# Kernel tuning notes

Measured on AMD Instinct MI355X. Metric: run time of the kernel, lower is better.

The kernel has to match this reference:

```python
import jax, jax.numpy as jnp
import numpy as np

K = 8192
D = 512


def setup_inputs() -> dict:
    key = jax.random.key(0)
    k1, k2 = jax.random.split(key)
    x = jax.random.normal(k1, (32, 512, D), dtype=jnp.float32)
    # nn.Embedding weight init: uniform(-1/k, 1/k)
    codebook = jax.random.uniform(k2, (K, D), dtype=jnp.float32,
                                  minval=-1.0 / K, maxval=1.0 / K)
    return {"x": x, "codebook": codebook}


def reference(x, codebook):
    # flatten to [N, D]
    z_e = x.reshape(-1, x.shape[-1])
    # squared L2 distances: ||z||^2 - 2 z c^T + ||c||^2  -> [N, K]
    dists = (jnp.sum(z_e * z_e, axis=1, keepdims=True)
             - 2.0 * jnp.einsum('nd,kd->nk', z_e, codebook)
             + jnp.sum(codebook * codebook, axis=1)[None, :])
    indices = jnp.argmin(dists, axis=1)  # [N]
    z_q = codebook[indices]              # [N, D] gather
    # straight-through estimator: forward z_q, grad passes to z_e
    z_q_st = z_e + jax.lax.stop_gradient(z_q - z_e)
    # vq loss pulls codebook toward (detached) encoder outputs
    vq_loss = jnp.mean((z_q - jax.lax.stop_gradient(z_e)) ** 2)
    # commitment loss pulls encoder outputs toward (detached) codes
    commit_loss = jnp.mean((z_e - jax.lax.stop_gradient(z_q)) ** 2)
    z_q_out = z_q_st.reshape(x.shape)
    idx_out = indices.reshape(x.shape[:-1])
    return z_q_out, vq_loss, commit_loss, idx_out
```

## Files before the change

kernel.cpp:

```cpp
#include <hip/hip_runtime.h>

#define K_CODES 8192
#define D_DIM   512
#define N_ROWS  16384
#define NSPLIT  32
#define CAP     8
#define T2      2.0e-4f
#define LIST_CAP 32768

typedef __attribute__((ext_vector_type(8))) short bf16x8;
typedef __attribute__((ext_vector_type(4))) float f32x4;
typedef unsigned char uchar;
typedef unsigned short ushort;
typedef unsigned long long u64;

__device__ __forceinline__ unsigned fkey(float f) {
    unsigned b = __float_as_uint(f);
    return (b & 0x80000000u) ? ~b : (b | 0x80000000u);
}
__device__ __forceinline__ float finv(unsigned k) {
    return __uint_as_float((k & 0x80000000u) ? (k & 0x7fffffffu) : ~k);
}

__device__ __forceinline__ unsigned pk_bf16(float a, float b) {
    unsigned ua = __float_as_uint(a), ub = __float_as_uint(b);
    ua = (ua + 0x7fffu + ((ua >> 16) & 1u)) >> 16;
    ub = (ub + 0x7fffu + ((ub >> 16) & 1u)) & 0xffff0000u;
    return ua | ub;
}

__global__ void vq_prepass(const float* __restrict__ x, const float* __restrict__ cb,
                           unsigned* __restrict__ xb, unsigned* __restrict__ cbb,
                           float* __restrict__ sn, u64* __restrict__ keys,
                           int* __restrict__ count) {
    const int bid = blockIdx.x;
    const int t = threadIdx.x;
    if (bid < 6144) {
        const size_t gid = (size_t)bid * 256 + t;
        const size_t nx = (size_t)N_ROWS * D_DIM / 8;
        if (gid < nx) {
            const float4 f0 = ((const float4*)x)[gid * 2];
            const float4 f1 = ((const float4*)x)[gid * 2 + 1];
            ((uint4*)xb)[gid] = make_uint4(pk_bf16(f0.x, f0.y), pk_bf16(f0.z, f0.w),
                                           pk_bf16(f1.x, f1.y), pk_bf16(f1.z, f1.w));
        } else {
            const size_t g = gid - nx;
            const float4 f0 = ((const float4*)cb)[g * 2];
            const float4 f1 = ((const float4*)cb)[g * 2 + 1];
            ((uint4*)cbb)[g] = make_uint4(pk_bf16(f0.x, f0.y), pk_bf16(f0.z, f0.w),
                                          pk_bf16(f1.x, f1.y), pk_bf16(f1.z, f1.w));
        }
    } else {
        const int base = (bid - 6144) * 8;
        if (bid == 6144 && t == 0) *count = 0;
        if (t < 8) keys[base + t] = ~0ull;
        const int wave = t >> 6, lane = t & 63;
        const int row = base + wave * 2 + (lane >> 5);
        const int l = lane & 31, b = l >> 3, j = l & 7;
        const float* a = x + (size_t)row * D_DIM + b * 128 + j;
        float r = __fmul_rn(a[0], a[0]);
#pragma unroll
        for (int i = 1; i < 16; ++i) {
            const float v = a[i * 8];
            r = __fadd_rn(r, __fmul_rn(v, v));
        }
        r = __fadd_rn(r, __shfl_xor(r, 1));
        r = __fadd_rn(r, __shfl_xor(r, 2));
        r = __fadd_rn(r, __shfl_xor(r, 4));
        r = __fadd_rn(r, __shfl_xor(r, 8));
        r = __fadd_rn(r, __shfl_xor(r, 16));
        if (l == 0) sn[row] = r;
    }
}

__global__ __launch_bounds__(256)
void vq_sn(const float* __restrict__ x, float* __restrict__ sn,
           u64* __restrict__ keys, int* __restrict__ count) {
    const int t = threadIdx.x;
    const int base = blockIdx.x * 8;
    if (blockIdx.x == 0 && t == 0) *count = 0;
    if (t < 8) keys[base + t] = ~0ull;
    const int wave = t >> 6, lane = t & 63;
    const int row = base + wave * 2 + (lane >> 5);
    const int l = lane & 31, b = l >> 3, j = l & 7;
    const float* a = x + (size_t)row * D_DIM + b * 128 + j;
    float r = __fmul_rn(a[0], a[0]);
#pragma unroll
    for (int i = 1; i < 16; ++i) {
        const float v = a[i * 8];
        r = __fadd_rn(r, __fmul_rn(v, v));
    }
    r = __fadd_rn(r, __shfl_xor(r, 1));
    r = __fadd_rn(r, __shfl_xor(r, 2));
    r = __fadd_rn(r, __shfl_xor(r, 4));
    r = __fadd_rn(r, __shfl_xor(r, 8));
    r = __fadd_rn(r, __shfl_xor(r, 16));
    if (l == 0) sn[row] = r;
}

template<bool PRE>
__global__ __launch_bounds__(256, 2)
void vq_screen2(const float* __restrict__ x, const float* __restrict__ cb,
                const ushort* __restrict__ xb, const ushort* __restrict__ cbb,
                float* __restrict__ g_dmax, uchar* __restrict__ g_cnt,
                uchar* __restrict__ g_cand) {
    __shared__ ushort Ash[128 * 32];
    __shared__ ushort Bsh[256 * 32];
    __shared__ unsigned vkey[128];
    __shared__ int ccnt[128];
    __shared__ uchar clist[128][CAP];

    const int t    = threadIdx.x;
    const int w    = t >> 6, lane = t & 63;
    const int fr   = lane & 15;
    const int quad = lane >> 4;
    const int wr   = (w & 1) * 64;
    const int wc   = (w >> 1) * 128;
    const int row0  = blockIdx.y * 128;
    const int kbase = blockIdx.x * 256;

    if (t < 128) { vkey[t] = 0u; ccnt[t] = 0; }

    const int r = t >> 1, h = t & 1;
    const int sA = (r >> 1) & 3;
    const int ca0 = (2 * h) ^ sA;
    ushort* awp0 = &Ash[r * 32 + ca0 * 8];
    ushort* awp1 = &Ash[r * 32 + (ca0 ^ 1) * 8];
    const int sB = (t >> 1) & 3;
    ushort* bwp0 = &Bsh[t * 32 + (0 ^ sB) * 8];
    ushort* bwp1 = &Bsh[t * 32 + (1 ^ sB) * 8];
    ushort* bwp2 = &Bsh[t * 32 + (2 ^ sB) * 8];
    ushort* bwp3 = &Bsh[t * 32 + (3 ^ sB) * 8];

    int aoff[4], boff[8];
#pragma unroll
    for (int i = 0; i < 4; ++i) {
        const int rw = wr + i * 16 + fr;
        aoff[i] = rw * 32 + ((quad ^ (rw >> 1)) & 3) * 8;
    }
#pragma unroll
    for (int j = 0; j < 8; ++j) {
        const int rw = wc + j * 16 + fr;
        boff[j] = rw * 32 + ((quad ^ (rw >> 1)) & 3) * 8;
    }

    f32x4 acc[4][8];
#pragma unroll
    for (int i = 0; i < 4; ++i)
#pragma unroll
        for (int j = 0; j < 8; ++j) acc[i][j] = (f32x4)0.0f;

    if (PRE) {
        const char* gA = (const char*)(xb  + (size_t)(row0 + r) * D_DIM + h * 16);
        const char* gB = (const char*)(cbb + (size_t)(kbase + t) * D_DIM);
        uint4 a0 = *(const uint4*)(gA);
        uint4 a1 = *(const uint4*)(gA + 16);
        uint4 b0 = *(const uint4*)(gB);
        uint4 b1 = *(const uint4*)(gB + 16);
        uint4 b2 = *(const uint4*)(gB + 32);
        uint4 b3 = *(const uint4*)(gB + 48);
        for (int dc = 0; dc < 16; ++dc) {
            __syncthreads();
            *(uint4*)awp0 = a0; *(uint4*)awp1 = a1;
            *(uint4*)bwp0 = b0; *(uint4*)bwp1 = b1;
            *(uint4*)bwp2 = b2; *(uint4*)bwp3 = b3;
            const int dn = (dc + 1) & 15;
            a0 = *(const uint4*)(gA + dn * 64);
            a1 = *(const uint4*)(gA + dn * 64 + 16);
            b0 = *(const uint4*)(gB + dn * 64);
            b1 = *(const uint4*)(gB + dn * 64 + 16);
            b2 = *(const uint4*)(gB + dn * 64 + 32);
            b3 = *(const uint4*)(gB + dn * 64 + 48);
            __syncthreads();
            bf16x8 af[4], bfv[8];
#pragma unroll
            for (int i = 0; i < 4; ++i) af[i] = *(const bf16x8*)&Ash[aoff[i]];
#pragma unroll
            for (int j = 0; j < 8; ++j) bfv[j] = *(const bf16x8*)&Bsh[boff[j]];
#pragma unroll
            for (int i = 0; i < 4; ++i)
#pragma unroll
                for (int j = 0; j < 8; ++j)
                    acc[i][j] = __builtin_amdgcn_mfma_f32_16x16x32_bf16(af[i], bfv[j], acc[i][j], 0, 0, 0);
        }
    } else {
        const char* gA = (const char*)(x  + (size_t)(row0 + r) * D_DIM + h * 16);
        const char* gB = (const char*)(cb + (size_t)(kbase + t) * D_DIM);
        for (int dc = 0; dc < 16; ++dc) {
            const float4* fa = (const float4*)(gA + dc * 128);
            float4 f0 = fa[0], f1 = fa[1], f2 = fa[2], f3 = fa[3];
            uint4 a0 = make_uint4(pk_bf16(f0.x, f0.y), pk_bf16(f0.z, f0.w),
                                  pk_bf16(f1.x, f1.y), pk_bf16(f1.z, f1.w));
            uint4 a1 = make_uint4(pk_bf16(f2.x, f2.y), pk_bf16(f2.z, f2.w),
                                  pk_bf16(f3.x, f3.y), pk_bf16(f3.z, f3.w));
            const float4* fb = (const float4*)(gB + dc * 128);
            float4 g0 = fb[0], g1 = fb[1], g2 = fb[2], g3 = fb[3];
            float4 g4 = fb[4], g5 = fb[5], g6 = fb[6], g7 = fb[7];
            uint4 b0 = make_uint4(pk_bf16(g0.x, g0.y), pk_bf16(g0.z, g0.w),
                                  pk_bf16(g1.x, g1.y), pk_bf16(g1.z, g1.w));
            uint4 b1 = make_uint4(pk_bf16(g2.x, g2.y), pk_bf16(g2.z, g2.w),
                                  pk_bf16(g3.x, g3.y), pk_bf16(g3.z, g3.w));
            uint4 b2 = make_uint4(pk_bf16(g4.x, g4.y), pk_bf16(g4.z, g4.w),
                                  pk_bf16(g5.x, g5.y), pk_bf16(g5.z, g5.w));
            uint4 b3 = make_uint4(pk_bf16(g6.x, g6.y), pk_bf16(g6.z, g6.w),
                                  pk_bf16(g7.x, g7.y), pk_bf16(g7.z, g7.w));
            __syncthreads();
            *(uint4*)awp0 = a0; *(uint4*)awp1 = a1;
            *(uint4*)bwp0 = b0; *(uint4*)bwp1 = b1;
            *(uint4*)bwp2 = b2; *(uint4*)bwp3 = b3;
            __syncthreads();
            bf16x8 af[4], bfv[8];
#pragma unroll
            for (int i = 0; i < 4; ++i) af[i] = *(const bf16x8*)&Ash[aoff[i]];
#pragma unroll
            for (int j = 0; j < 8; ++j) bfv[j] = *(const bf16x8*)&Bsh[boff[j]];
#pragma unroll
            for (int i = 0; i < 4; ++i)
#pragma unroll
                for (int j = 0; j < 8; ++j)
                    acc[i][j] = __builtin_amdgcn_mfma_f32_16x16x32_bf16(af[i], bfv[j], acc[i][j], 0, 0, 0);
        }
    }

    __syncthreads();
#pragma unroll
    for (int i = 0; i < 4; ++i)
#pragma unroll
        for (int rg = 0; rg < 4; ++rg) {
            float m = acc[i][0][rg];
#pragma unroll
            for (int j = 1; j < 8; ++j) m = fmaxf(m, acc[i][j][rg]);
            m = fmaxf(m, __shfl_xor(m, 1));
            m = fmaxf(m, __shfl_xor(m, 2));
            m = fmaxf(m, __shfl_xor(m, 4));
            m = fmaxf(m, __shfl_xor(m, 8));
            if (fr == 0) atomicMax(&vkey[wr + i * 16 + quad * 4 + rg], fkey(m));
        }
    __syncthreads();
#pragma unroll
    for (int i = 0; i < 4; ++i)
#pragma unroll
        for (int rg = 0; rg < 4; ++rg) {
            const int row = wr + i * 16 + quad * 4 + rg;
            const float thr = finv(vkey[row]) - T2;
#pragma unroll
            for (int j = 0; j < 8; ++j) {
                if (acc[i][j][rg] >= thr) {
                    int p = atomicAdd(&ccnt[row], 1);
                    if (p < CAP) clist[row][p] = (uchar)(wc + j * 16 + fr);
                }
            }
        }
    __syncthreads();
    if (t < 128) {
        const size_t o = (size_t)(row0 + t) * NSPLIT + blockIdx.x;
        g_dmax[o] = finv(vkey[t]);
        int c = ccnt[t];
        g_cnt[o] = (uchar)(c > 255 ? 255 : c);
        ((uint2*)g_cand)[o] = *(const uint2*)clist[t];
    }
}

__global__ __launch_bounds__(256)
void vq_build(const float* __restrict__ g_dmax, const uchar* __restrict__ g_cnt,
              const uchar* __restrict__ g_cand, int2* __restrict__ list,
              int* __restrict__ count, float* __restrict__ idx_f) {
    const int row = blockIdx.x * blockDim.x + threadIdx.x;
    const int lane = threadIdx.x & 63;
    const float* dm = g_dmax + (size_t)row * NSPLIT;
    float g = dm[0];
#pragma unroll
    for (int s = 1; s < NSPLIT; ++s) g = fmaxf(g, dm[s]);
    const float thr = g - T2;

    int tot = 0, first = -1;
    for (int s = 0; s < NSPLIT; ++s) {
        if (dm[s] < thr) continue;
        const size_t o = (size_t)row * NSPLIT + s;
        const int c = g_cnt[o];
        tot += (c > CAP) ? 256 : c;
        if (first < 0) first = s * 256 + g_cand[o * CAP];
    }
    idx_f[row] = (float)first;

    const int need = (tot > 1) ? tot : 0;
    int scan = need;
#pragma unroll
    for (int d = 1; d < 64; d <<= 1) {
        const int v = __shfl_up(scan, d, 64);
        if (lane >= d) scan += v;
    }
    const int wtot = __shfl(scan, 63, 64);
    int base = 0;
    if (lane == 63 && wtot > 0) base = atomicAdd(count, wtot);
    base = __shfl(base, 63, 64);
    if (need == 0) return;
    int pos = base + scan - need;

    for (int s = 0; s < NSPLIT; ++s) {
        if (dm[s] < thr) continue;
        const size_t o = (size_t)row * NSPLIT + s;
        const int c = g_cnt[o];
        if (c > CAP) {
            for (int u = 0; u < 256; ++u, ++pos)
                if (pos < LIST_CAP) list[pos] = make_int2(row, s * 256 + u);
        } else {
            for (int u = 0; u < c; ++u, ++pos)
                if (pos < LIST_CAP) list[pos] = make_int2(row, s * 256 + g_cand[o * CAP + u]);
        }
    }
}

__device__ __forceinline__ float np_einsum_dot(const float* __restrict__ a,
                                               const float* __restrict__ b) {
    float S0 = 0.f, S1 = 0.f, S2 = 0.f, S3 = 0.f;
    for (int i = 0; i < D_DIM; i += 16) {
        S0 = __fadd_rn(S0, __fmul_rn(a[i + 12], b[i + 12]));
        S1 = __fadd_rn(S1, __fmul_rn(a[i + 13], b[i + 13]));
        S2 = __fadd_rn(S2, __fmul_rn(a[i + 14], b[i + 14]));
        S3 = __fadd_rn(S3, __fmul_rn(a[i + 15], b[i + 15]));
        S0 = __fadd_rn(S0, __fmul_rn(a[i +  8], b[i +  8]));
        S1 = __fadd_rn(S1, __fmul_rn(a[i +  9], b[i +  9]));
        S2 = __fadd_rn(S2, __fmul_rn(a[i + 10], b[i + 10]));
        S3 = __fadd_rn(S3, __fmul_rn(a[i + 11], b[i + 11]));
        S0 = __fadd_rn(S0, __fmul_rn(a[i +  4], b[i +  4]));
        S1 = __fadd_rn(S1, __fmul_rn(a[i +  5], b[i +  5]));
        S2 = __fadd_rn(S2, __fmul_rn(a[i +  6], b[i +  6]));
        S3 = __fadd_rn(S3, __fmul_rn(a[i +  7], b[i +  7]));
        S0 = __fadd_rn(S0, __fmul_rn(a[i +  0], b[i +  0]));
        S1 = __fadd_rn(S1, __fmul_rn(a[i +  1], b[i +  1]));
        S2 = __fadd_rn(S2, __fmul_rn(a[i +  2], b[i +  2]));
        S3 = __fadd_rn(S3, __fmul_rn(a[i +  3], b[i +  3]));
    }
    return __fadd_rn(__fadd_rn(S0, S1), __fadd_rn(S2, S3));
}

__global__ __launch_bounds__(256)
void vq_replay(const float* __restrict__ x, const float* __restrict__ cb,
               const float* __restrict__ sn, const int2* __restrict__ list,
               const int* __restrict__ count, u64* __restrict__ keys) {
    const int i = blockIdx.x * blockDim.x + threadIdx.x;
    int n = *count; if (n > LIST_CAP) n = LIST_CAP;
    if (i >= n) return;
    const int2 e = list[i];
    const float* zr = x + (size_t)e.x * D_DIM;
    const float d = __fadd_rn(sn[e.x],
                              __fmul_rn(-2.0f, np_einsum_dot(zr, cb + (size_t)e.y * D_DIM)));
    const u64 key = ((u64)fkey(d) << 32) | (unsigned)e.y;
    atomicMin(&keys[e.x], key);
}

__global__ void vq_gather_kernel(const float* __restrict__ x,
                                 const float* __restrict__ cb,
                                 const u64* __restrict__ keys,
                                 float* __restrict__ idx_f,
                                 float* __restrict__ zq_out,
                                 double* __restrict__ psum) {
    const int row = blockIdx.x;
    const int t   = threadIdx.x;
    const u64 ky = keys[row];
    const int k = (ky != ~0ull) ? (int)(ky & 0xffffffffu) : (int)idx_f[row];
    const float4 c  = ((const float4*)(cb + (size_t)k   * D_DIM))[t];
    const float4 xv = ((const float4*)(x  + (size_t)row * D_DIM))[t];
    float4 o;
    o.x = __fadd_rn(xv.x, __fsub_rn(c.x, xv.x));
    o.y = __fadd_rn(xv.y, __fsub_rn(c.y, xv.y));
    o.z = __fadd_rn(xv.z, __fsub_rn(c.z, xv.z));
    o.w = __fadd_rn(xv.w, __fsub_rn(c.w, xv.w));
    ((float4*)(zq_out + (size_t)row * D_DIM))[t] = o;
    const double d0 = (double)c.x - (double)xv.x;
    const double d1 = (double)c.y - (double)xv.y;
    const double d2 = (double)c.z - (double)xv.z;
    const double d3 = (double)c.w - (double)xv.w;
    double s = d0 * d0 + d1 * d1 + d2 * d2 + d3 * d3;
#pragma unroll
    for (int off = 32; off > 0; off >>= 1) s += __shfl_xor(s, off, 64);
    __shared__ double red[2];
    if ((t & 63) == 0) red[t >> 6] = s;
    __syncthreads();
    if (t == 0) {
        psum[row] = red[0] + red[1];
        idx_f[row] = (float)k;
    }
}

__global__ void vq_finalize2(const double* __restrict__ psum,
                             float* __restrict__ losses) {
    __shared__ double red[4];
    const int t = threadIdx.x;
    double s = 0.0;
    for (int i = t; i < N_ROWS; i += 256) s += psum[i];
#pragma unroll
    for (int off = 32; off > 0; off >>= 1) s += __shfl_xor(s, off, 64);
    if ((t & 63) == 0) red[t >> 6] = s;
    __syncthreads();
    if (t == 0) {
        const double tot = red[0] + red[1] + red[2] + red[3];
        const float l = (float)(tot / (double)((size_t)N_ROWS * D_DIM));
        losses[0] = l;
        losses[1] = l;
    }
}

extern "C" void kernel_launch(void* const* d_in, const int* in_sizes, int n_in,
                              void* d_out, int out_size, void* d_ws, size_t ws_size,
                              hipStream_t stream) {
    const float* x  = (const float*)d_in[0];
    const float* cb = (const float*)d_in[1];
    float* out    = (float*)d_out;
    float* zq     = out;
    float* losses = out + (size_t)N_ROWS * D_DIM;
    float* idx_f  = losses + 2;
    char* ws = (char*)d_ws;

    const bool pre = (ws_size >= ((size_t)32 << 20));
    char* base = pre ? (ws + ((size_t)24 << 20)) : ws;

    float*  g_dmax = (float*)(base);
    uchar*  g_cnt  = (uchar*)(base + (2048u << 10));
    uchar*  g_cand = (uchar*)(base + (2560u << 10));
    float*  sn     = (float*)(base + (6656u << 10));
    u64*    keys   = (u64*)  (base + (6720u << 10));
    int2*   list   = (int2*) (base + (6848u << 10));
    int*    count  = (int*)  (base + (7104u << 10));
    double* psum   = (double*)(base + (7168u << 10));

    if (pre) {
        ushort* xb  = (ushort*)ws;
        ushort* cbb = (ushort*)(ws + ((size_t)16 << 20));
        hipLaunchKernelGGL(vq_prepass, dim3(8192), dim3(256), 0, stream,
                           x, cb, (unsigned*)xb, (unsigned*)cbb, sn, keys, count);
        hipLaunchKernelGGL((vq_screen2<true>), dim3(K_CODES / 256, N_ROWS / 128), dim3(256), 0, stream,
                           x, cb, xb, cbb, g_dmax, g_cnt, g_cand);
    } else {
        hipLaunchKernelGGL(vq_sn, dim3(N_ROWS / 8), dim3(256), 0, stream,
                           x, sn, keys, count);
        hipLaunchKernelGGL((vq_screen2<false>), dim3(K_CODES / 256, N_ROWS / 128), dim3(256), 0, stream,
                           x, cb, (const ushort*)nullptr, (const ushort*)nullptr,
                           g_dmax, g_cnt, g_cand);
    }
    hipLaunchKernelGGL(vq_build, dim3(N_ROWS / 256), dim3(256), 0, stream,
                       g_dmax, g_cnt, g_cand, list, count, idx_f);
    hipLaunchKernelGGL(vq_replay, dim3(LIST_CAP / 256), dim3(256), 0, stream,
                       x, cb, sn, list, count, keys);
    hipLaunchKernelGGL(vq_gather_kernel, dim3(N_ROWS), dim3(128), 0, stream,
                       x, cb, keys, idx_f, zq, psum);
    hipLaunchKernelGGL(vq_finalize2, dim3(1), dim3(256), 0, stream,
                       psum, losses);
}
```

Baseline: 396.8 us.

## Double-buffer LDS in bf16 screen GEMM and fuse build/replay/gather/finalize tail

```diff
diff --git a/kernel.cpp b/kernel.cpp
--- a/kernel.cpp
+++ b/kernel.cpp
@@ -6,7 +6,6 @@
 #define NSPLIT  32
 #define CAP     8
 #define T2      2.0e-4f
-#define LIST_CAP 32768
 
 typedef __attribute__((ext_vector_type(8))) short bf16x8;
 typedef __attribute__((ext_vector_type(4))) float f32x4;
@@ -14,6 +13,8 @@
 typedef unsigned short ushort;
 typedef unsigned long long u64;
 
+#define BAR_LDS() asm volatile("s_waitcnt lgkmcnt(0)\n\ts_barrier" ::: "memory")
+
 __device__ __forceinline__ unsigned fkey(float f) {
     unsigned b = __float_as_uint(f);
     return (b & 0x80000000u) ? ~b : (b | 0x80000000u);
@@ -31,8 +32,7 @@
 
 __global__ void vq_prepass(const float* __restrict__ x, const float* __restrict__ cb,
                            unsigned* __restrict__ xb, unsigned* __restrict__ cbb,
-                           float* __restrict__ sn, u64* __restrict__ keys,
-                           int* __restrict__ count) {
+                           float* __restrict__ sn, int* __restrict__ done) {
     const int bid = blockIdx.x;
     const int t = threadIdx.x;
     if (bid < 6144) {
@@ -52,8 +52,7 @@
         }
     } else {
         const int base = (bid - 6144) * 8;
-        if (bid == 6144 && t == 0) *count = 0;
-        if (t < 8) keys[base + t] = ~0ull;
+        if (bid == 6144 && t == 0) *done = 0;
         const int wave = t >> 6, lane = t & 63;
         const int row = base + wave * 2 + (lane >> 5);
         const int l = lane & 31, b = l >> 3, j = l & 7;
@@ -75,11 +74,10 @@
 
 __global__ __launch_bounds__(256)
 void vq_sn(const float* __restrict__ x, float* __restrict__ sn,
-           u64* __restrict__ keys, int* __restrict__ count) {
+           int* __restrict__ done) {
     const int t = threadIdx.x;
     const int base = blockIdx.x * 8;
-    if (blockIdx.x == 0 && t == 0) *count = 0;
-    if (t < 8) keys[base + t] = ~0ull;
+    if (blockIdx.x == 0 && t == 0) *done = 0;
     const int wave = t >> 6, lane = t & 63;
     const int row = base + wave * 2 + (lane >> 5);
     const int l = lane & 31, b = l >> 3, j = l & 7;
@@ -98,12 +96,143 @@
     if (l == 0) sn[row] = r;
 }
 
-template<bool PRE>
 __global__ __launch_bounds__(256, 2)
-void vq_screen2(const float* __restrict__ x, const float* __restrict__ cb,
-                const ushort* __restrict__ xb, const ushort* __restrict__ cbb,
-                float* __restrict__ g_dmax, uchar* __restrict__ g_cnt,
-                uchar* __restrict__ g_cand) {
+void vq_screen_pre(const ushort* __restrict__ xb, const ushort* __restrict__ cbb,
+                   float* __restrict__ g_dmax, uchar* __restrict__ g_cnt,
+                   uchar* __restrict__ g_cand) {
+    __shared__ ushort Ash[2][128 * 32];
+    __shared__ ushort Bsh[2][256 * 32];
+    __shared__ unsigned vkey[128];
+    __shared__ int ccnt[128];
+    __shared__ uchar clist[128][CAP];
+
+    const int t    = threadIdx.x;
+    const int w    = t >> 6, lane = t & 63;
+    const int fr   = lane & 15;
+    const int quad = lane >> 4;
+    const int wr   = (w & 1) * 64;
+    const int wc   = (w >> 1) * 128;
+    const int row0  = blockIdx.y * 128;
+    const int kbase = blockIdx.x * 256;
+
+    if (t < 128) { vkey[t] = 0u; ccnt[t] = 0; }
+
+    const int r = t >> 1, h = t & 1;
+    const int sA = (r >> 1) & 3;
+    const int ca0 = (2 * h) ^ sA;
+    const int aw0 = r * 32 + ca0 * 8;
+    const int aw1 = r * 32 + (ca0 ^ 1) * 8;
+    const int sB = (t >> 1) & 3;
+    const int bw0 = t * 32 + (0 ^ sB) * 8;
+    const int bw1 = t * 32 + (1 ^ sB) * 8;
+    const int bw2 = t * 32 + (2 ^ sB) * 8;
+    const int bw3 = t * 32 + (3 ^ sB) * 8;
+
+    int aoff[4], boff[8];
+#pragma unroll
+    for (int i = 0; i < 4; ++i) {
+        const int rw = wr + i * 16 + fr;
+        aoff[i] = rw * 32 + ((quad ^ (rw >> 1)) & 3) * 8;
+    }
+#pragma unroll
+    for (int j = 0; j < 8; ++j) {
+        const int rw = wc + j * 16 + fr;
+        boff[j] = rw * 32 + ((quad ^ (rw >> 1)) & 3) * 8;
+    }
+
+    const char* gA = (const char*)(xb  + (size_t)(row0 + r) * D_DIM + h * 16);
+    const char* gB = (const char*)(cbb + (size_t)(kbase + t) * D_DIM);
+
+    f32x4 acc[4][8];
+#pragma unroll
+    for (int i = 0; i < 4; ++i)
+#pragma unroll
+        for (int j = 0; j < 8; ++j) acc[i][j] = (f32x4)0.0f;
+
+    uint4 a0 = *(const uint4*)(gA);
+    uint4 a1 = *(const uint4*)(gA + 16);
+    uint4 b0 = *(const uint4*)(gB);
+    uint4 b1 = *(const uint4*)(gB + 16);
+    uint4 b2 = *(const uint4*)(gB + 32);
+    uint4 b3 = *(const uint4*)(gB + 48);
+    *(uint4*)&Ash[0][aw0] = a0; *(uint4*)&Ash[0][aw1] = a1;
+    *(uint4*)&Bsh[0][bw0] = b0; *(uint4*)&Bsh[0][bw1] = b1;
+    *(uint4*)&Bsh[0][bw2] = b2; *(uint4*)&Bsh[0][bw3] = b3;
+    a0 = *(const uint4*)(gA + 64);
+    a1 = *(const uint4*)(gA + 64 + 16);
+    b0 = *(const uint4*)(gB + 64);
+    b1 = *(const uint4*)(gB + 64 + 16);
+    b2 = *(const uint4*)(gB + 64 + 32);
+    b3 = *(const uint4*)(gB + 64 + 48);
+    BAR_LDS();
+
+    for (int dc = 0; dc < 16; ++dc) {
+        const int p = dc & 1;
+        bf16x8 af[4], bfv[8];
+#pragma unroll
+        for (int i = 0; i < 4; ++i) af[i] = *(const bf16x8*)&Ash[p][aoff[i]];
+#pragma unroll
+        for (int j = 0; j < 8; ++j) bfv[j] = *(const bf16x8*)&Bsh[p][boff[j]];
+        *(uint4*)&Ash[p ^ 1][aw0] = a0; *(uint4*)&Ash[p ^ 1][aw1] = a1;
+        *(uint4*)&Bsh[p ^ 1][bw0] = b0; *(uint4*)&Bsh[p ^ 1][bw1] = b1;
+        *(uint4*)&Bsh[p ^ 1][bw2] = b2; *(uint4*)&Bsh[p ^ 1][bw3] = b3;
+        const int dn = (dc + 2) & 15;
+        a0 = *(const uint4*)(gA + dn * 64);
+        a1 = *(const uint4*)(gA + dn * 64 + 16);
+        b0 = *(const uint4*)(gB + dn * 64);
+        b1 = *(const uint4*)(gB + dn * 64 + 16);
+        b2 = *(const uint4*)(gB + dn * 64 + 32);
+        b3 = *(const uint4*)(gB + dn * 64 + 48);
+#pragma unroll
+        for (int i = 0; i < 4; ++i)
+#pragma unroll
+            for (int j = 0; j < 8; ++j)
+                acc[i][j] = __builtin_amdgcn_mfma_f32_16x16x32_bf16(af[i], bfv[j], acc[i][j], 0, 0, 0);
+        BAR_LDS();
+    }
+
+#pragma unroll
+    for (int i = 0; i < 4; ++i)
+#pragma unroll
+        for (int rg = 0; rg < 4; ++rg) {
+            float m = acc[i][0][rg];
+#pragma unroll
+            for (int j = 1; j < 8; ++j) m = fmaxf(m, acc[i][j][rg]);
+            m = fmaxf(m, __shfl_xor(m, 1));
+            m = fmaxf(m, __shfl_xor(m, 2));
+            m = fmaxf(m, __shfl_xor(m, 4));
+            m = fmaxf(m, __shfl_xor(m, 8));
+            if (fr == 0) atomicMax(&vkey[wr + i * 16 + quad * 4 + rg], fkey(m));
+        }
+    __syncthreads();
+#pragma unroll
+    for (int i = 0; i < 4; ++i)
+#pragma unroll
+        for (int rg = 0; rg < 4; ++rg) {
+            const int row = wr + i * 16 + quad * 4 + rg;
+            const float thr = finv(vkey[row]) - T2;
+#pragma unroll
+            for (int j = 0; j < 8; ++j) {
+                if (acc[i][j][rg] >= thr) {
+                    int p = atomicAdd(&ccnt[row], 1);
+                    if (p < CAP) clist[row][p] = (uchar)(wc + j * 16 + fr);
+                }
+            }
+        }
+    __syncthreads();
+    if (t < 128) {
+        const size_t o = (size_t)(row0 + t) * NSPLIT + blockIdx.x;
+        g_dmax[o] = finv(vkey[t]);
+        int c = ccnt[t];
+        g_cnt[o] = (uchar)(c > 255 ? 255 : c);
+        ((uint2*)g_cand)[o] = *(const uint2*)clist[t];
+    }
+}
+
+__global__ __launch_bounds__(256, 2)
+void vq_screen_np(const float* __restrict__ x, const float* __restrict__ cb,
+                  float* __restrict__ g_dmax, uchar* __restrict__ g_cnt,
+                  uchar* __restrict__ g_cand) {
     __shared__ ushort Ash[128 * 32];
     __shared__ ushort Bsh[256 * 32];
     __shared__ unsigned vkey[128];
@@ -150,76 +279,41 @@
 #pragma unroll
         for (int j = 0; j < 8; ++j) acc[i][j] = (f32x4)0.0f;
 
-    if (PRE) {
-        const char* gA = (const char*)(xb  + (size_t)(row0 + r) * D_DIM + h * 16);
-        const char* gB = (const char*)(cbb + (size_t)(kbase + t) * D_DIM);
-        uint4 a0 = *(const uint4*)(gA);
-        uint4 a1 = *(const uint4*)(gA + 16);
-        uint4 b0 = *(const uint4*)(gB);
-        uint4 b1 = *(const uint4*)(gB + 16);
-        uint4 b2 = *(const uint4*)(gB + 32);
-        uint4 b3 = *(const uint4*)(gB + 48);
-        for (int dc = 0; dc < 16; ++dc) {
-            __syncthreads();
-            *(uint4*)awp0 = a0; *(uint4*)awp1 = a1;
-            *(uint4*)bwp0 = b0; *(uint4*)bwp1 = b1;
-            *(uint4*)bwp2 = b2; *(uint4*)bwp3 = b3;
-            const int dn = (dc + 1) & 15;
-            a0 = *(const uint4*)(gA + dn * 64);
-            a1 = *(const uint4*)(gA + dn * 64 + 16);
-            b0 = *(const uint4*)(gB + dn * 64);
-            b1 = *(const uint4*)(gB + dn * 64 + 16);
-            b2 = *(const uint4*)(gB + dn * 64 + 32);
-            b3 = *(const uint4*)(gB + dn * 64 + 48);
-            __syncthreads();
-            bf16x8 af[4], bfv[8];
-#pragma unroll
-            for (int i = 0; i < 4; ++i) af[i] = *(const bf16x8*)&Ash[aoff[i]];
-#pragma unroll
-            for (int j = 0; j < 8; ++j) bfv[j] = *(const bf16x8*)&Bsh[boff[j]];
-#pragma unroll
-            for (int i = 0; i < 4; ++i)
-#pragma unroll
-                for (int j = 0; j < 8; ++j)
-                    acc[i][j] = __builtin_amdgcn_mfma_f32_16x16x32_bf16(af[i], bfv[j], acc[i][j], 0, 0, 0);
-        }
-    } else {
-        const char* gA = (const char*)(x  + (size_t)(row0 + r) * D_DIM + h * 16);
-        const char* gB = (const char*)(cb + (size_t)(kbase + t) * D_DIM);
-        for (int dc = 0; dc < 16; ++dc) {
-            const float4* fa = (const float4*)(gA + dc * 128);
-            float4 f0 = fa[0], f1 = fa[1], f2 = fa[2], f3 = fa[3];
-            uint4 a0 = make_uint4(pk_bf16(f0.x, f0.y), pk_bf16(f0.z, f0.w),
-                                  pk_bf16(f1.x, f1.y), pk_bf16(f1.z, f1.w));
-            uint4 a1 = make_uint4(pk_bf16(f2.x, f2.y), pk_bf16(f2.z, f2.w),
-                                  pk_bf16(f3.x, f3.y), pk_bf16(f3.z, f3.w));
-            const float4* fb = (const float4*)(gB + dc * 128);
-            float4 g0 = fb[0], g1 = fb[1], g2 = fb[2], g3 = fb[3];
-            float4 g4 = fb[4], g5 = fb[5], g6 = fb[6], g7 = fb[7];
-            uint4 b0 = make_uint4(pk_bf16(g0.x, g0.y), pk_bf16(g0.z, g0.w),
-                                  pk_bf16(g1.x, g1.y), pk_bf16(g1.z, g1.w));
-            uint4 b1 = make_uint4(pk_bf16(g2.x, g2.y), pk_bf16(g2.z, g2.w),
-                                  pk_bf16(g3.x, g3.y), pk_bf16(g3.z, g3.w));
-            uint4 b2 = make_uint4(pk_bf16(g4.x, g4.y), pk_bf16(g4.z, g4.w),
-                                  pk_bf16(g5.x, g5.y), pk_bf16(g5.z, g5.w));
-            uint4 b3 = make_uint4(pk_bf16(g6.x, g6.y), pk_bf16(g6.z, g6.w),
-                                  pk_bf16(g7.x, g7.y), pk_bf16(g7.z, g7.w));
-            __syncthreads();
-            *(uint4*)awp0 = a0; *(uint4*)awp1 = a1;
-            *(uint4*)bwp0 = b0; *(uint4*)bwp1 = b1;
-            *(uint4*)bwp2 = b2; *(uint4*)bwp3 = b3;
-            __syncthreads();
-            bf16x8 af[4], bfv[8];
-#pragma unroll
-            for (int i = 0; i < 4; ++i) af[i] = *(const bf16x8*)&Ash[aoff[i]];
-#pragma unroll
-            for (int j = 0; j < 8; ++j) bfv[j] = *(const bf16x8*)&Bsh[boff[j]];
-#pragma unroll
-            for (int i = 0; i < 4; ++i)
-#pragma unroll
-                for (int j = 0; j < 8; ++j)
-                    acc[i][j] = __builtin_amdgcn_mfma_f32_16x16x32_bf16(af[i], bfv[j], acc[i][j], 0, 0, 0);
-        }
+    const char* gA = (const char*)(x  + (size_t)(row0 + r) * D_DIM + h * 16);
+    const char* gB = (const char*)(cb + (size_t)(kbase + t) * D_DIM);
+    for (int dc = 0; dc < 16; ++dc) {
+        const float4* fa = (const float4*)(gA + dc * 128);
+        float4 f0 = fa[0], f1 = fa[1], f2 = fa[2], f3 = fa[3];
+        uint4 a0 = make_uint4(pk_bf16(f0.x, f0.y), pk_bf16(f0.z, f0.w),
+                              pk_bf16(f1.x, f1.y), pk_bf16(f1.z, f1.w));
+        uint4 a1 = make_uint4(pk_bf16(f2.x, f2.y), pk_bf16(f2.z, f2.w),
+                              pk_bf16(f3.x, f3.y), pk_bf16(f3.z, f3.w));
+        const float4* fb = (const float4*)(gB + dc * 128);
+        float4 g0 = fb[0], g1 = fb[1], g2 = fb[2], g3 = fb[3];
+        float4 g4 = fb[4], g5 = fb[5], g6 = fb[6], g7 = fb[7];
+        uint4 b0 = make_uint4(pk_bf16(g0.x, g0.y), pk_bf16(g0.z, g0.w),
+                              pk_bf16(g1.x, g1.y), pk_bf16(g1.z, g1.w));
+        uint4 b1 = make_uint4(pk_bf16(g2.x, g2.y), pk_bf16(g2.z, g2.w),
+                              pk_bf16(g3.x, g3.y), pk_bf16(g3.z, g3.w));
+        uint4 b2 = make_uint4(pk_bf16(g4.x, g4.y), pk_bf16(g4.z, g4.w),
+                              pk_bf16(g5.x, g5.y), pk_bf16(g5.z, g5.w));
+        uint4 b3 = make_uint4(pk_bf16(g6.x, g6.y), pk_bf16(g6.z, g6.w),
+                              pk_bf16(g7.x, g7.y), pk_bf16(g7.z, g7.w));
+        __syncthreads();
+        *(uint4*)awp0 = a0; *(uint4*)awp1 = a1;
+        *(uint4*)bwp0 = b0; *(uint4*)bwp1 = b1;
+        *(uint4*)bwp2 = b2; *(uint4*)bwp3 = b3;
+        __syncthreads();
+        bf16x8 af[4], bfv[8];
+#pragma unroll
+        for (int i = 0; i < 4; ++i) af[i] = *(const bf16x8*)&Ash[aoff[i]];
+#pragma unroll
+        for (int j = 0; j < 8; ++j) bfv[j] = *(const bf16x8*)&Bsh[boff[j]];
+#pragma unroll
+        for (int i = 0; i < 4; ++i)
+#pragma unroll
+            for (int j = 0; j < 8; ++j)
+                acc[i][j] = __builtin_amdgcn_mfma_f32_16x16x32_bf16(af[i], bfv[j], acc[i][j], 0, 0, 0);
     }
 
     __syncthreads();
@@ -258,56 +352,6 @@
         int c = ccnt[t];
         g_cnt[o] = (uchar)(c > 255 ? 255 : c);
         ((uint2*)g_cand)[o] = *(const uint2*)clist[t];
-    }
-}
-
-__global__ __launch_bounds__(256)
-void vq_build(const float* __restrict__ g_dmax, const uchar* __restrict__ g_cnt,
-              const uchar* __restrict__ g_cand, int2* __restrict__ list,
-              int* __restrict__ count, float* __restrict__ idx_f) {
-    const int row = blockIdx.x * blockDim.x + threadIdx.x;
-    const int lane = threadIdx.x & 63;
-    const float* dm = g_dmax + (size_t)row * NSPLIT;
-    float g = dm[0];
-#pragma unroll
-    for (int s = 1; s < NSPLIT; ++s) g = fmaxf(g, dm[s]);
-    const float thr = g - T2;
-
-    int tot = 0, first = -1;
-    for (int s = 0; s < NSPLIT; ++s) {
-        if (dm[s] < thr) continue;
-        const size_t o = (size_t)row * NSPLIT + s;
-        const int c = g_cnt[o];
-        tot += (c > CAP) ? 256 : c;
-        if (first < 0) first = s * 256 + g_cand[o * CAP];
-    }
-    idx_f[row] = (float)first;
-
-    const int need = (tot > 1) ? tot : 0;
-    int scan = need;
-#pragma unroll
-    for (int d = 1; d < 64; d <<= 1) {
-        const int v = __shfl_up(scan, d, 64);
-        if (lane >= d) scan += v;
-    }
-    const int wtot = __shfl(scan, 63, 64);
-    int base = 0;
-    if (lane == 63 && wtot > 0) base = atomicAdd(count, wtot);
-    base = __shfl(base, 63, 64);
-    if (need == 0) return;
-    int pos = base + scan - need;
-
-    for (int s = 0; s < NSPLIT; ++s) {
-        if (dm[s] < thr) continue;
-        const size_t o = (size_t)row * NSPLIT + s;
-        const int c = g_cnt[o];
-        if (c > CAP) {
-            for (int u = 0; u < 256; ++u, ++pos)
-                if (pos < LIST_CAP) list[pos] = make_int2(row, s * 256 + u);
-        } else {
-            for (int u = 0; u < c; ++u, ++pos)
-                if (pos < LIST_CAP) list[pos] = make_int2(row, s * 256 + g_cand[o * CAP + u]);
-        }
     }
 }
 
@@ -335,70 +379,124 @@
     return __fadd_rn(__fadd_rn(S0, S1), __fadd_rn(S2, S3));
 }
 
-__global__ __launch_bounds__(256)
-void vq_replay(const float* __restrict__ x, const float* __restrict__ cb,
-               const float* __restrict__ sn, const int2* __restrict__ list,
-               const int* __restrict__ count, u64* __restrict__ keys) {
-    const int i = blockIdx.x * blockDim.x + threadIdx.x;
-    int n = *count; if (n > LIST_CAP) n = LIST_CAP;
-    if (i >= n) return;
-    const int2 e = list[i];
-    const float* zr = x + (size_t)e.x * D_DIM;
-    const float d = __fadd_rn(sn[e.x],
-                              __fmul_rn(-2.0f, np_einsum_dot(zr, cb + (size_t)e.y * D_DIM)));
-    const u64 key = ((u64)fkey(d) << 32) | (unsigned)e.y;
-    atomicMin(&keys[e.x], key);
-}
-
-__global__ void vq_gather_kernel(const float* __restrict__ x,
-                                 const float* __restrict__ cb,
-                                 const u64* __restrict__ keys,
-                                 float* __restrict__ idx_f,
-                                 float* __restrict__ zq_out,
-                                 double* __restrict__ psum) {
+__global__ __launch_bounds__(128)
+void vq_tail(const float* __restrict__ x, const float* __restrict__ cb,
+             const float* __restrict__ sn_arr, const float* __restrict__ g_dmax,
+             const uchar* __restrict__ g_cnt, const uchar* __restrict__ g_cand,
+             float* __restrict__ idx_f, float* __restrict__ zq,
+             double* __restrict__ psum, int* __restrict__ done,
+             float* __restrict__ losses) {
     const int row = blockIdx.x;
-    const int t   = threadIdx.x;
-    const u64 ky = keys[row];
-    const int k = (ky != ~0ull) ? (int)(ky & 0xffffffffu) : (int)idx_f[row];
-    const float4 c  = ((const float4*)(cb + (size_t)k   * D_DIM))[t];
+    const int t = threadIdx.x, lane = t & 63, wv = t >> 6;
+    __shared__ u64 s_red[2];
+    __shared__ double s_ls[2];
+    __shared__ int s_last;
+
+    const float* dm = g_dmax + (size_t)row * NSPLIT;
+    float g = dm[lane & 31];
+    g = fmaxf(g, __shfl_xor(g, 1));
+    g = fmaxf(g, __shfl_xor(g, 2));
+    g = fmaxf(g, __shfl_xor(g, 4));
+    g = fmaxf(g, __shfl_xor(g, 8));
+    g = fmaxf(g, __shfl_xor(g, 16));
+    const float thr = g - T2;
+
+    int contr = 0;
+    unsigned firstkey = 0xffffffffu;
+    if (lane < 32) {
+        if (dm[lane] >= thr) {
+            const size_t o = (size_t)row * NSPLIT + lane;
+            const int c = g_cnt[o];
+            contr = (c > CAP) ? 256 : c;
+            firstkey = ((unsigned)lane << 16) | (unsigned)(lane * 256 + g_cand[o * CAP]);
+        }
+    }
+    int tot = contr;
+    unsigned fk = firstkey;
+#pragma unroll
+    for (int off = 1; off < 64; off <<= 1) {
+        tot += __shfl_xor(tot, off);
+        fk = min(fk, (unsigned)__shfl_xor((int)fk, off));
+    }
+
+    int k;
+    if (tot <= 1) {
+        k = (int)(fk & 0xffffu);
+    } else {
+        const float* zr = x + (size_t)row * D_DIM;
+        const float sn = sn_arr[row];
+        u64 best = ~0ull;
+        for (int s = 0; s < NSPLIT; ++s) {
+            if (dm[s] < thr) continue;
+            const size_t o = (size_t)row * NSPLIT + s;
+            const int c = g_cnt[o];
+            if (c <= CAP) {
+                if (t < c) {
+                    const int kk = s * 256 + g_cand[o * CAP + t];
+                    const float e = np_einsum_dot(zr, cb + (size_t)kk * D_DIM);
+                    const float d = __fadd_rn(sn, __fmul_rn(-2.0f, e));
+                    const u64 key = ((u64)fkey(d) << 32) | (unsigned)kk;
+                    best = best < key ? best : key;
+                }
+            } else {
+#pragma unroll
+                for (int u = 0; u < 2; ++u) {
+                    const int kk = s * 256 + t + u * 128;
+                    const float e = np_einsum_dot(zr, cb + (size_t)kk * D_DIM);
+                    const float d = __fadd_rn(sn, __fmul_rn(-2.0f, e));
+                    const u64 key = ((u64)fkey(d) << 32) | (unsigned)kk;
+                    best = best < key ? best : key;
+                }
+            }
+        }
+#pragma unroll
+        for (int off = 1; off < 64; off <<= 1) {
+            const u64 o2 = __shfl_xor(best, off);
+            best = best < o2 ? best : o2;
+        }
+        if (lane == 0) s_red[wv] = best;
+        __syncthreads();
+        const u64 b2 = s_red[0] < s_red[1] ? s_red[0] : s_red[1];
+        k = (int)(b2 & 0xffffffffu);
+    }
+
+    const float4 c4 = ((const float4*)(cb + (size_t)k   * D_DIM))[t];
     const float4 xv = ((const float4*)(x  + (size_t)row * D_DIM))[t];
     float4 o;
-    o.x = __fadd_rn(xv.x, __fsub_rn(c.x, xv.x));
-    o.y = __fadd_rn(xv.y, __fsub_rn(c.y, xv.y));
-    o.z = __fadd_rn(xv.z, __fsub_rn(c.z, xv.z));
-    o.w = __fadd_rn(xv.w, __fsub_rn(c.w, xv.w));
-    ((float4*)(zq_out + (size_t)row * D_DIM))[t] = o;
-    const double d0 = (double)c.x - (double)xv.x;
-    const double d1 = (double)c.y - (double)xv.y;
-    const double d2 = (double)c.z - (double)xv.z;
-    const double d3 = (double)c.w - (double)xv.w;
+    o.x = __fadd_rn(xv.x, __fsub_rn(c4.x, xv.x));
+    o.y = __fadd_rn(xv.y, __fsub_rn(c4.y, xv.y));
+    o.z = __fadd_rn(xv.z, __fsub_rn(c4.z, xv.z));
+    o.w = __fadd_rn(xv.w, __fsub_rn(c4.w, xv.w));
+    ((float4*)(zq + (size_t)row * D_DIM))[t] = o;
+    const double d0 = (double)c4.x - (double)xv.x;
+    const double d1 = (double)c4.y - (double)xv.y;
+    const double d2 = (double)c4.z - (double)xv.z;
+    const double d3 = (double)c4.w - (double)xv.w;
     double s = d0 * d0 + d1 * d1 + d2 * d2 + d3 * d3;
 #pragma unroll
     for (int off = 32; off > 0; off >>= 1) s += __shfl_xor(s, off, 64);
-    __shared__ double red[2];
-    if ((t & 63) == 0) red[t >> 6] = s;
+    if (lane == 0) s_ls[wv] = s;
     __syncthreads();
     if (t == 0) {
-        psum[row] = red[0] + red[1];
+        psum[row] = s_ls[0] + s_ls[1];
         idx_f[row] = (float)k;
-    }
-}
-
-__global__ void vq_finalize2(const double* __restrict__ psum,
-                             float* __restrict__ losses) {
-    __shared__ double red[4];
-    const int t = threadIdx.x;
-    double s = 0.0;
-    for (int i = t; i < N_ROWS; i += 256) s += psum[i];
-#pragma unroll
-    for (int off = 32; off > 0; off >>= 1) s += __shfl_xor(s, off, 64);
-    if ((t & 63) == 0) red[t >> 6] = s;
-    __syncthreads();
-    if (t == 0) {
-        const double tot = red[0] + red[1] + red[2] + red[3];
-        const float l = (float)(tot / (double)((size_t)N_ROWS * D_DIM));
-        losses[0] = l;
-        losses[1] = l;
+        __threadfence();
+        s_last = (atomicAdd(done, 1) == N_ROWS - 1);
+    }
+    __syncthreads();
+    if (s_last) {
+        __threadfence();
+        double s2 = 0.0;
+        for (int i = t; i < N_ROWS; i += 128) s2 += psum[i];
+#pragma unroll
+        for (int off = 32; off > 0; off >>= 1) s2 += __shfl_xor(s2, off, 64);
+        if (lane == 0) s_ls[wv] = s2;
+        __syncthreads();
+        if (t == 0) {
+            const float l = (float)((s_ls[0] + s_ls[1]) / (double)((size_t)N_ROWS * D_DIM));
+            losses[0] = l;
+            losses[1] = l;
+        }
     }
 }
 
@@ -420,31 +518,22 @@
     uchar*  g_cnt  = (uchar*)(base + (2048u << 10));
     uchar*  g_cand = (uchar*)(base + (2560u << 10));
     float*  sn     = (float*)(base + (6656u << 10));
-    u64*    keys   = (u64*)  (base + (6720u << 10));
-    int2*   list   = (int2*) (base + (6848u << 10));
-    int*    count  = (int*)  (base + (7104u << 10));
-    double* psum   = (double*)(base + (7168u << 10));
+    double* psum   = (double*)(base + (6720u << 10));
+    int*    done   = (int*)  (base + (6848u << 10));
 
     if (pre) {
         ushort* xb  = (ushort*)ws;
         ushort* cbb = (ushort*)(ws + ((size_t)16 << 20));
         hipLaunchKernelGGL(vq_prepass, dim3(8192), dim3(256), 0, stream,
-                           x, cb, (unsigned*)xb, (unsigned*)cbb, sn, keys, count);
-        hipLaunchKernelGGL((vq_screen2<true>), dim3(K_CODES / 256, N_ROWS / 128), dim3(256), 0, stream,
-                           x, cb, xb, cbb, g_dmax, g_cnt, g_cand);
+                           x, cb, (unsigned*)xb, (unsigned*)cbb, sn, done);
+        hipLaunchKernelGGL(vq_screen_pre, dim3(K_CODES / 256, N_ROWS / 128), dim3(256), 0, stream,
+                           xb, cbb, g_dmax, g_cnt, g_cand);
     } else {
         hipLaunchKernelGGL(vq_sn, dim3(N_ROWS / 8), dim3(256), 0, stream,
-                           x, sn, keys, count);
-        hipLaunchKernelGGL((vq_screen2<false>), dim3(K_CODES / 256, N_ROWS / 128), dim3(256), 0, stream,
-                           x, cb, (const ushort*)nullptr, (const ushort*)nullptr,
-                           g_dmax, g_cnt, g_cand);
-    }
-    hipLaunchKernelGGL(vq_build, dim3(N_ROWS / 256), dim3(256), 0, stream,
-                       g_dmax, g_cnt, g_cand, list, count, idx_f);
-    hipLaunchKernelGGL(vq_replay, dim3(LIST_CAP / 256), dim3(256), 0, stream,
-                       x, cb, sn, list, count, keys);
-    hipLaunchKernelGGL(vq_gather_kernel, dim3(N_ROWS), dim3(128), 0, stream,
-                       x, cb, keys, idx_f, zq, psum);
-    hipLaunchKernelGGL(vq_finalize2, dim3(1), dim3(256), 0, stream,
-                       psum, losses);
-}
+                           x, sn, done);
+        hipLaunchKernelGGL(vq_screen_np, dim3(K_CODES / 256, N_ROWS / 128), dim3(256), 0, stream,
+                           x, cb, g_dmax, g_cnt, g_cand);
+    }
+    hipLaunchKernelGGL(vq_tail, dim3(N_ROWS), dim3(128), 0, stream,
+                       x, cb, sn, g_dmax, g_cnt, g_cand, idx_f, zq, psum, done, losses);
+}
```

Result: slower. 842.9 us (+112.4%).
